# Performance work log

Hardware: AMD Instinct MI355X
Metric: run time of the kernel (lower is better)

Reference implementation:

```python
import jax, jax.numpy as jnp
import numpy as np

NUM_HEADS = 24
EPS = 1e-6


def rms_norm(x, scale):
    # fp32 RMSNorm over last dim, matching torch F.rms_norm(eps=1e-6)
    xf = x.astype(jnp.float32)
    rrms = jax.lax.rsqrt(jnp.mean(xf * xf, axis=-1, keepdims=True) + EPS)
    return (xf * rrms * scale.astype(jnp.float32)).astype(x.dtype)


def rope_rotate(x, pe):
    # x: [B,H,L,D]; pe: [B,1,L,D/2,2,2] rotation matrices
    B, H, L, D = x.shape
    xr = x.astype(jnp.float32).reshape(B, H, L, D // 2, 1, 2)
    out = pe[..., 0] * xr[..., 0] + pe[..., 1] * xr[..., 1]  # [B,H,L,D/2,2]
    return out.reshape(B, H, L, D).astype(x.dtype)


def setup_inputs() -> dict:
    key = jax.random.key(0)
    ks = jax.random.split(key, 6)
    B, L, C = 1, 2048, 3072
    H = NUM_HEADS
    D = C // H
    x = jax.random.normal(ks[0], (B, L, C), dtype=jnp.float32)
    # pe: proper RoPE rotation matrices [[cos,-sin],[sin,cos]] -> [B,1,L,D/2,2,2]
    theta = jax.random.uniform(ks[1], (B, 1, L, D // 2), dtype=jnp.float32) * (2.0 * np.pi)
    cos, sin = jnp.cos(theta), jnp.sin(theta)
    row0 = jnp.stack([cos, -sin], axis=-1)
    row1 = jnp.stack([sin, cos], axis=-1)
    pe = jnp.stack([row0, row1], axis=-2)  # [B,1,L,D/2,2,2]
    w_qkv = jax.random.normal(ks[2], (3 * C, C), dtype=jnp.float32) * (1.0 / np.sqrt(C))
    q_scale = jnp.ones((D,), dtype=jnp.float32)
    k_scale = jnp.ones((D,), dtype=jnp.float32)
    w_proj = jax.random.normal(ks[3], (C, C), dtype=jnp.float32) * (1.0 / np.sqrt(C))
    b_proj = jnp.zeros((C,), dtype=jnp.float32)
    return {"x": x, "pe": pe, "w_qkv": w_qkv, "q_scale": q_scale,
            "k_scale": k_scale, "w_proj": w_proj, "b_proj": b_proj}


def reference(x, pe, w_qkv, q_scale, k_scale, w_proj, b_proj):
    B, L, C = x.shape
    H = NUM_HEADS
    D = C // H
    qkv = x @ w_qkv.T                                   # [B,L,3C]
    qkv = qkv.reshape(B, L, 3, H, D).transpose(2, 0, 3, 1, 4)  # [3,B,H,L,D]
    q, k, v = qkv[0], qkv[1], qkv[2]
    q = rms_norm(q, q_scale)
    k = rms_norm(k, k_scale)
    q = rope_rotate(q, pe)
    k = rope_rotate(k, pe)
    scale = 1.0 / np.sqrt(D)
    scores = jnp.einsum('bhqd,bhkd->bhqk', q, k) * jnp.asarray(scale, q.dtype)
    attn = jax.nn.softmax(scores, axis=-1)
    out = jnp.einsum('bhqk,bhkd->bhqd', attn, v)        # [B,H,L,D]
    out = out.transpose(0, 2, 1, 3).reshape(B, L, C)    # [B,L,C]
    return out @ w_proj.T + b_proj
```

## Files before the change

### kernel.cpp

```cpp
#include <hip/hip_runtime.h>

typedef __attribute__((ext_vector_type(8))) __bf16 bf16x8;
typedef __attribute__((ext_vector_type(4))) float f32x4;

typedef __attribute__((address_space(1))) void gvoid;
typedef __attribute__((address_space(3))) void lvoid;

__device__ __forceinline__ float bf2f(unsigned int u) {
    union { unsigned int u; float f; } v; v.u = u << 16; return v.f;
}
__device__ __forceinline__ unsigned short f2bf(float f) {
    union { float f; unsigned int u; } v; v.f = f;
    unsigned int r = v.u + 0x7fffu + ((v.u >> 16) & 1u);
    return (unsigned short)(r >> 16);
}
__device__ __forceinline__ unsigned int pack2(float a, float b) {
    return (unsigned int)f2bf(a) | ((unsigned int)f2bf(b) << 16);
}
__device__ __forceinline__ void async16(const void* g, void* l) {
    __builtin_amdgcn_global_load_lds((gvoid*)g, (lvoid*)l, 16, 0, 0);
}
__device__ __forceinline__ float exp2f_hw(float x) {
    return __builtin_amdgcn_exp2f(x);
}


__global__ __launch_bounds__(256)
void cvt_all(const float4* __restrict__ x, const float4* __restrict__ wqkv,
             const float4* __restrict__ wproj, uint4* __restrict__ dst) {
    int i = blockIdx.x * 256 + threadIdx.x;
    const float4* s; uint4* d; int off;
    if (i < 786432)       { s = x;     d = dst;           off = i; }
    else if (i < 4325376) { s = wqkv;  d = dst + 786432;  off = i - 786432; }
    else if (i < 5505024) { s = wproj; d = dst + 4325376; off = i - 4325376; }
    else return;
    float4 a = s[2 * off], b = s[2 * off + 1];
    uint4 o;
    o.x = pack2(a.x, a.y); o.y = pack2(a.z, a.w);
    o.z = pack2(b.x, b.y); o.w = pack2(b.z, b.w);
    d[off] = o;
}

#define GEMM_CORE(A_, lda_, B_, ldb_, K_)                                        \
    __shared__ __align__(16) unsigned short As[4][4096];                         \
    __shared__ __align__(16) unsigned short Bs[4][4096];                         \
    const int t = threadIdx.x, lane = t & 63;                                    \
    const int wm = t >> 7, wn = (t >> 6) & 1;                                    \
    const int lr = lane & 15, kc = lane >> 4;                                    \
    const int NK = (K_) / 32;                                                    \
    const int e0 = t * 8, e1 = (256 + t) * 8;                                    \
    const int r0 = e0 >> 5, c0 = (e0 >> 3) & 3;                                  \
    const int r1 = e1 >> 5, c1 = (e1 >> 3) & 3;                                  \
    const int g0 = (c0 ^ ((r0 >> 1) & 3)) * 8;                                   \
    const int g1 = (c1 ^ ((r1 >> 1) & 3)) * 8;                                   \
    const unsigned short* Ag0 = &(A_)[(size_t)(m0 + r0) * (lda_) + g0];          \
    const unsigned short* Ag1 = &(A_)[(size_t)(m0 + r1) * (lda_) + g1];          \
    const unsigned short* Bg0 = &(B_)[(size_t)(n0 + r0) * (ldb_) + g0];          \
    const unsigned short* Bg1 = &(B_)[(size_t)(n0 + r1) * (ldb_) + g1];          \
    f32x4 acc[4][4] = {};                                                        \
    RSTAGE(0) RSTAGE(1) RSTAGE(2)                                                \
    asm volatile("s_waitcnt vmcnt(8)" ::: "memory");                             \
    __builtin_amdgcn_s_barrier();                                                \
    for (int kt = 0; kt < NK; ++kt) {                                            \
        const int sl = kt & 3;                                                   \
        bf16x8 af[4], bfr[4];                                                    \
        _Pragma("unroll")                                                        \
        for (int i = 0; i < 4; ++i) {                                            \
            int ra = wm * 64 + i * 16 + lr;                                      \
            int rb = wn * 64 + i * 16 + lr;                                      \
            af[i]  = *(const bf16x8*)&As[sl][ra * 32 + ((kc ^ ((ra >> 1) & 3)) * 8)]; \
            bfr[i] = *(const bf16x8*)&Bs[sl][rb * 32 + ((kc ^ ((rb >> 1) & 3)) * 8)]; \
        }                                                                        \
        if (kt + 3 < NK) RSTAGE(kt + 3)                                          \
        asm volatile("s_waitcnt lgkmcnt(0)" ::: "memory");                       \
        __builtin_amdgcn_sched_barrier(0);                                       \
        __builtin_amdgcn_s_setprio(1);                                           \
        _Pragma("unroll")                                                        \
        for (int mi = 0; mi < 4; ++mi)                                           \
            _Pragma("unroll")                                                    \
            for (int ni = 0; ni < 4; ++ni)                                       \
                acc[mi][ni] = __builtin_amdgcn_mfma_f32_16x16x32_bf16(           \
                    af[mi], bfr[ni], acc[mi][ni], 0, 0, 0);                      \
        __builtin_amdgcn_s_setprio(0);                                           \
        if (kt + 3 < NK)      { asm volatile("s_waitcnt vmcnt(8)" ::: "memory"); } \
        else if (kt + 2 < NK) { asm volatile("s_waitcnt vmcnt(4)" ::: "memory"); } \
        else if (kt + 1 < NK) { asm volatile("s_waitcnt vmcnt(0)" ::: "memory"); } \
        __builtin_amdgcn_s_barrier();                                            \
    }

#define RSTAGE(kt_) { const int s_ = (kt_) & 3; const size_t k_ = (size_t)(kt_) * 32; \
        async16(Ag0 + k_, &As[s_][e0]); async16(Ag1 + k_, &As[s_][e1]);               \
        async16(Bg0 + k_, &Bs[s_][e0]); async16(Bg1 + k_, &Bs[s_][e1]); }

__global__ __launch_bounds__(256, 2)
void gemm_qkv(const unsigned short* __restrict__ A, const unsigned short* __restrict__ B,
              unsigned short* __restrict__ qk, unsigned short* __restrict__ vt) {
    __shared__ __align__(16) unsigned short As[3][4096];
    __shared__ __align__(16) unsigned short Bs[3][8192];
    const int n0 = blockIdx.x * 256, m0 = blockIdx.y * 128;
    const int t = threadIdx.x, lane = t & 63, w = t >> 6;
    const int lr = lane & 15, kc = lane >> 4;
    const int NK = 96;

    const int ea0 = t * 8,         ra0 = ea0 >> 5, ca0 = (ea0 >> 3) & 3;
    const int ea1 = (256 + t) * 8, ra1 = ea1 >> 5, ca1 = (ea1 >> 3) & 3;
    const int ga0 = (ca0 ^ ((ra0 >> 1) & 3)) * 8;
    const int ga1 = (ca1 ^ ((ra1 >> 1) & 3)) * 8;
    const unsigned short* Ag0 = &A[(size_t)(m0 + ra0) * 3072 + ga0];
    const unsigned short* Ag1 = &A[(size_t)(m0 + ra1) * 3072 + ga1];
    int eb[4];
    const unsigned short* Bg[4];
#pragma unroll
    for (int i = 0; i < 4; ++i) {
        eb[i] = (i * 256 + t) * 8;
        int rb = eb[i] >> 5, cb = (eb[i] >> 3) & 3;
        int gb = (cb ^ ((rb >> 1) & 3)) * 8;
        Bg[i] = &B[(size_t)(n0 + rb) * 3072 + gb];
    }

#define QSTAGE(kt_) { const int s_ = (kt_) % 3; const size_t k_ = (size_t)(kt_) * 32; \
        async16(Ag0 + k_, &As[s_][ea0]); async16(Ag1 + k_, &As[s_][ea1]);             \
        async16(Bg[0] + k_, &Bs[s_][eb[0]]); async16(Bg[1] + k_, &Bs[s_][eb[1]]);     \
        async16(Bg[2] + k_, &Bs[s_][eb[2]]); async16(Bg[3] + k_, &Bs[s_][eb[3]]); }

    f32x4 acc[8][4] = {};

    QSTAGE(0) QSTAGE(1)
    asm volatile("s_waitcnt vmcnt(6)" ::: "memory");
    __builtin_amdgcn_s_barrier();

    for (int kt = 0; kt < NK; ++kt) {
        const int sl = kt % 3;
        bf16x8 af[8], bfr[4];
#pragma unroll
        for (int i = 0; i < 8; ++i) {
            int ra = i * 16 + lr;
            af[i] = *(const bf16x8*)&As[sl][ra * 32 + ((kc ^ ((ra >> 1) & 3)) * 8)];
        }
#pragma unroll
        for (int i = 0; i < 4; ++i) {
            int rb = w * 64 + i * 16 + lr;
            bfr[i] = *(const bf16x8*)&Bs[sl][rb * 32 + ((kc ^ ((rb >> 1) & 3)) * 8)];
        }
        if (kt + 2 < NK) QSTAGE(kt + 2)
        asm volatile("s_waitcnt lgkmcnt(0)" ::: "memory");
        __builtin_amdgcn_sched_barrier(0);
        __builtin_amdgcn_s_setprio(1);
#pragma unroll
        for (int mi = 0; mi < 8; ++mi)
#pragma unroll
            for (int ni = 0; ni < 4; ++ni)
                acc[mi][ni] = __builtin_amdgcn_mfma_f32_16x16x32_bf16(
                    af[mi], bfr[ni], acc[mi][ni], 0, 0, 0);
        __builtin_amdgcn_s_setprio(0);
        if (kt + 2 < NK) { asm volatile("s_waitcnt vmcnt(6)" ::: "memory"); }
        else             { asm volatile("s_waitcnt vmcnt(0)" ::: "memory"); }
        __builtin_amdgcn_s_barrier();
    }
#undef QSTAGE

    const int rb0 = kc * 4;
#pragma unroll
    for (int mi = 0; mi < 8; ++mi)
#pragma unroll
        for (int ni = 0; ni < 4; ++ni) {
            int col = n0 + w * 64 + ni * 16 + lr;
#pragma unroll
            for (int r = 0; r < 4; ++r) {
                int row = m0 + mi * 16 + rb0 + r;
                unsigned short v = f2bf(acc[mi][ni][r]);
                if (col < 6144) qk[(size_t)row * 6144 + col] = v;
                else            vt[(size_t)(col - 6144) * 2048 + row] = v;
            }
        }
}

__global__ __launch_bounds__(256, 2)
void gemm_proj(const unsigned short* __restrict__ A, const unsigned short* __restrict__ B,
               const float* __restrict__ bias, float* __restrict__ out) {
    const int n0 = blockIdx.x * 128, m0 = blockIdx.y * 128;
    GEMM_CORE(A, 6144, B, 3072, 3072)
    const int rb0 = kc * 4;
#pragma unroll
    for (int mi = 0; mi < 4; ++mi)
#pragma unroll
        for (int ni = 0; ni < 4; ++ni) {
            int col = n0 + wn * 64 + ni * 16 + lr;
            float badd = bias[col];
#pragma unroll
            for (int r = 0; r < 4; ++r) {
                int row = m0 + wm * 64 + mi * 16 + rb0 + r;
                out[(size_t)row * 3072 + col] = acc[mi][ni][r] + badd;
            }
        }
}

__global__ __launch_bounds__(256, 2)
void attn2(unsigned short* __restrict__ qk, const unsigned short* __restrict__ vt) {
    __shared__ __align__(16) unsigned short Ks[64 * 128];
    __shared__ __align__(16) unsigned short Vs[128 * 64];
    __shared__ __align__(16) unsigned short Ps[4 * 32 * 64];
    const int t = threadIdx.x, lane = t & 63, w = t >> 6;
    const int h = blockIdx.x, qblk = blockIdx.y * 128;
    const int lr = lane & 15, kc = lane >> 4;
    const float sc2 = 0.08838834764831845f * 1.4426950408889634f;
    const float THR = 62.7f;

    bf16x8 aq[2][4];
#pragma unroll
    for (int mf = 0; mf < 2; ++mf)
#pragma unroll
        for (int ks = 0; ks < 4; ++ks)
            aq[mf][ks] = *(const bf16x8*)&qk[(size_t)(qblk + w * 32 + mf * 16 + lr) * 6144 + h * 128 + ks * 32 + kc * 8];

    f32x4 o[2][8] = {};
    float mst[2][4], lpart[2][4];
#pragma unroll
    for (int mf = 0; mf < 2; ++mf)
#pragma unroll
        for (int r = 0; r < 4; ++r) { mst[mf][r] = -1e30f; lpart[mf][r] = 0.0f; }

    unsigned short* Pw = &Ps[w * 2048];

#pragma unroll
    for (int i = 0; i < 4; ++i) {
        int e = (i * 256 + t) * 8;
        {
            int row = e >> 7, c8 = (e >> 3) & 15;
            int gc = (c8 ^ (row & 15)) * 8;
            async16(&qk[(size_t)row * 6144 + 3072 + h * 128 + gc], &Ks[e]);
        }
        {
            int row = e >> 6, c8 = (e >> 3) & 7;
            int gc = (c8 ^ (row & 7)) * 8;
            async16(&vt[(size_t)(h * 128 + row) * 2048 + gc], &Vs[e]);
        }
    }

    for (int kb = 0; kb < 2048; kb += 64) {
        __syncthreads();

        bf16x8 pk[4], pv[4];
        const bool pf = (kb + 64) < 2048;
        if (pf) {
#pragma unroll
            for (int i = 0; i < 4; ++i) {
                int e = (i * 256 + t) * 8;
                {   int row = e >> 7, c8 = (e >> 3) & 15;
                    int gc = (c8 ^ (row & 15)) * 8;
                    pk[i] = *(const bf16x8*)&qk[(size_t)(kb + 64 + row) * 6144 + 3072 + h * 128 + gc];
                }
                {   int row = e >> 6, c8 = (e >> 3) & 7;
                    int gc = (c8 ^ (row & 7)) * 8;
                    pv[i] = *(const bf16x8*)&vt[(size_t)(h * 128 + row) * 2048 + kb + 64 + gc];
                }
            }
        }

        f32x4 s[2][4] = {};
#pragma unroll
        for (int nt = 0; nt < 4; ++nt) {
            int rk = nt * 16 + lr;
#pragma unroll
            for (int ks = 0; ks < 4; ++ks) {
                int ck = ks * 4 + kc;
                bf16x8 bk = *(const bf16x8*)&Ks[rk * 128 + ((ck ^ (rk & 15)) * 8)];
#pragma unroll
                for (int mf = 0; mf < 2; ++mf)
                    s[mf][nt] = __builtin_amdgcn_mfma_f32_16x16x32_bf16(aq[mf][ks], bk, s[mf][nt], 0, 0, 0);
            }
        }

#pragma unroll
        for (int mf = 0; mf < 2; ++mf) {
            float lm[4]; bool need = false;
#pragma unroll
            for (int r = 0; r < 4; ++r) {
                lm[r] = fmaxf(fmaxf(s[mf][0][r], s[mf][1][r]), fmaxf(s[mf][2][r], s[mf][3][r]));
                need = need || (lm[r] > mst[mf][r] + THR);
            }
            if (__ballot(need) != 0ull) {
#pragma unroll
                for (int r = 0; r < 4; ++r) {
                    float vmax = lm[r];
#pragma unroll
                    for (int off = 8; off >= 1; off >>= 1) vmax = fmaxf(vmax, __shfl_xor(vmax, off));
                    float mn = fmaxf(mst[mf][r], vmax);
                    float al = exp2f_hw((mst[mf][r] - mn) * sc2);
                    mst[mf][r] = mn;
                    lpart[mf][r] *= al;
#pragma unroll
                    for (int dt = 0; dt < 8; ++dt) o[mf][dt][r] *= al;
                }
            }
#pragma unroll
            for (int r = 0; r < 4; ++r) {
                float ps = 0.0f;
#pragma unroll
                for (int nt = 0; nt < 4; ++nt) {
                    float p = exp2f_hw((s[mf][nt][r] - mst[mf][r]) * sc2);
                    s[mf][nt][r] = p;
                    ps += p;
                }
                lpart[mf][r] += ps;
            }
        }

#pragma unroll
        for (int mf = 0; mf < 2; ++mf)
#pragma unroll
            for (int nt = 0; nt < 4; ++nt) {
                int col = nt * 16 + lr;
                int chunk = col >> 3, cin = col & 7;
#pragma unroll
                for (int r = 0; r < 4; ++r) {
                    int q = mf * 16 + kc * 4 + r;
                    Pw[q * 64 + ((chunk ^ (q & 7)) * 8 + cin)] = f2bf(s[mf][nt][r]);
                }
            }

#pragma unroll
        for (int ks2 = 0; ks2 < 2; ++ks2) {
            int ck = ks2 * 4 + kc;
            bf16x8 ap[2];
#pragma unroll
            for (int mf = 0; mf < 2; ++mf) {
                int q = mf * 16 + lr;
                ap[mf] = *(const bf16x8*)&Pw[q * 64 + ((ck ^ (q & 7)) * 8)];
            }
#pragma unroll
            for (int dt = 0; dt < 8; ++dt) {
                int rv = dt * 16 + lr;
                bf16x8 bv = *(const bf16x8*)&Vs[rv * 64 + ((ck ^ (rv & 7)) * 8)];
#pragma unroll
                for (int mf = 0; mf < 2; ++mf)
                    o[mf][dt] = __builtin_amdgcn_mfma_f32_16x16x32_bf16(ap[mf], bv, o[mf][dt], 0, 0, 0);
            }
        }
        __syncthreads();

        if (pf) {
#pragma unroll
            for (int i = 0; i < 4; ++i) {
                int e = (i * 256 + t) * 8;
                *(bf16x8*)&Ks[e] = pk[i];
                *(bf16x8*)&Vs[e] = pv[i];
            }
        }
    }

#pragma unroll
    for (int mf = 0; mf < 2; ++mf)
#pragma unroll
        for (int r = 0; r < 4; ++r) {
            float ps = lpart[mf][r];
#pragma unroll
            for (int off = 8; off >= 1; off >>= 1) ps += __shfl_xor(ps, off);
            lpart[mf][r] = ps;
        }
#pragma unroll
    for (int mf = 0; mf < 2; ++mf)
#pragma unroll
        for (int dt = 0; dt < 8; ++dt)
#pragma unroll
            for (int r = 0; r < 4; ++r) {
                int row = qblk + w * 32 + mf * 16 + kc * 4 + r;
                qk[(size_t)row * 6144 + h * 128 + dt * 16 + lr] = f2bf(o[mf][dt][r] / lpart[mf][r]);
            }
}


__global__ __launch_bounds__(256)
void norm_rope(unsigned short* __restrict__ qk, const float* __restrict__ pe,
               const float* __restrict__ q_scale, const float* __restrict__ k_scale) {
    const int wid = threadIdx.x >> 6, lane = threadIdx.x & 63;
    int pid = blockIdx.x * 4 + wid;
    const int isK = pid >= 49152;
    int p2 = isK ? pid - 49152 : pid;
    const int h = p2 >> 11, l = p2 & 2047;

    unsigned short* src = qk + (size_t)l * 6144 + (isK ? 3072 : 0) + h * 128 + lane * 2;
    unsigned int xu = *(const unsigned int*)src;
    float x0 = bf2f(xu & 0xffffu), x1 = bf2f(xu >> 16);
    float ss = x0 * x0 + x1 * x1;
#pragma unroll
    for (int off = 32; off >= 1; off >>= 1) ss += __shfl_xor(ss, off);
    float rr = rsqrtf(ss * (1.0f / 128.0f) + 1e-6f);

    const float* sc = isK ? k_scale : q_scale;
    float2 s2 = *(const float2*)(sc + lane * 2);
    float y0 = x0 * rr * s2.x;
    float y1 = x1 * rr * s2.y;

    float4 p4 = *(const float4*)(pe + ((size_t)l * 64 + lane) * 4);
    float o0 = p4.x * y0 + p4.y * y1;
    float o1 = p4.z * y0 + p4.w * y1;

    *(unsigned int*)src = pack2(o0, o1);
}


template <bool A32, bool B32, bool C32, bool HAS_BIAS, bool TRANS_C>
__global__ __launch_bounds__(256, 2)
void gemm_bt(const void* __restrict__ Ap, const void* __restrict__ Bp,
             const float* __restrict__ bias, void* __restrict__ Cp,
             int M, int N, int K, int lda, int ldc) {
    __shared__ __align__(16) unsigned short As[128 * 40];
    __shared__ __align__(16) unsigned short Bs[128 * 40];
    const int t = threadIdx.x, lane = t & 63;
    const int wm = t >> 7, wn = (t >> 6) & 1;
    const int m0 = blockIdx.x * 128, n0 = blockIdx.y * 128;
    const int lr = lane & 15, kc = lane >> 4;
    f32x4 acc[4][4] = {};

    for (int k0 = 0; k0 < K; k0 += 32) {
        float4 ra32[4], rb32[4];
        bf16x8 ra16[2], rb16[2];
        if constexpr (A32) {
            const float* A = (const float*)Ap;
#pragma unroll
            for (int i = 0; i < 4; ++i) {
                int idx = i * 256 + t, row = idx >> 3, c4 = idx & 7;
                ra32[i] = *(const float4*)&A[(size_t)(m0 + row) * lda + k0 + c4 * 4];
            }
        } else {
            const unsigned short* A = (const unsigned short*)Ap;
#pragma unroll
            for (int i = 0; i < 2; ++i) {
                int idx = i * 256 + t, row = idx >> 2, c8 = idx & 3;
                ra16[i] = *(const bf16x8*)&A[(size_t)(m0 + row) * lda + k0 + c8 * 8];
            }
        }
        if constexpr (B32) {
            const float* B = (const float*)Bp;
#pragma unroll
            for (int i = 0; i < 4; ++i) {
                int idx = i * 256 + t, row = idx >> 3, c4 = idx & 7;
                rb32[i] = *(const float4*)&B[(size_t)(n0 + row) * K + k0 + c4 * 4];
            }
        } else {
            const unsigned short* B = (const unsigned short*)Bp;
#pragma unroll
            for (int i = 0; i < 2; ++i) {
                int idx = i * 256 + t, row = idx >> 2, c8 = idx & 3;
                rb16[i] = *(const bf16x8*)&B[(size_t)(n0 + row) * K + k0 + c8 * 8];
            }
        }
        __syncthreads();
        if constexpr (A32) {
#pragma unroll
            for (int i = 0; i < 4; ++i) {
                int idx = i * 256 + t, row = idx >> 3, c4 = idx & 7;
                uint2 p = { pack2(ra32[i].x, ra32[i].y), pack2(ra32[i].z, ra32[i].w) };
                *(uint2*)&As[row * 40 + c4 * 4] = p;
            }
        } else {
#pragma unroll
            for (int i = 0; i < 2; ++i) {
                int idx = i * 256 + t, row = idx >> 2, c8 = idx & 3;
                *(bf16x8*)&As[row * 40 + c8 * 8] = ra16[i];
            }
        }
        if constexpr (B32) {
#pragma unroll
            for (int i = 0; i < 4; ++i) {
                int idx = i * 256 + t, row = idx >> 3, c4 = idx & 7;
                uint2 p = { pack2(rb32[i].x, rb32[i].y), pack2(rb32[i].z, rb32[i].w) };
                *(uint2*)&Bs[row * 40 + c4 * 4] = p;
            }
        } else {
#pragma unroll
            for (int i = 0; i < 2; ++i) {
                int idx = i * 256 + t, row = idx >> 2, c8 = idx & 3;
                *(bf16x8*)&Bs[row * 40 + c8 * 8] = rb16[i];
            }
        }
        __syncthreads();
        bf16x8 af[4], bfr[4];
#pragma unroll
        for (int i = 0; i < 4; ++i) {
            af[i]  = *(const bf16x8*)&As[(wm * 64 + i * 16 + lr) * 40 + kc * 8];
            bfr[i] = *(const bf16x8*)&Bs[(wn * 64 + i * 16 + lr) * 40 + kc * 8];
        }
#pragma unroll
        for (int mi = 0; mi < 4; ++mi)
#pragma unroll
            for (int ni = 0; ni < 4; ++ni)
                acc[mi][ni] = __builtin_amdgcn_mfma_f32_16x16x32_bf16(af[mi], bfr[ni], acc[mi][ni], 0, 0, 0);
    }
    const int rb0 = kc * 4;
#pragma unroll
    for (int mi = 0; mi < 4; ++mi) {
#pragma unroll
        for (int ni = 0; ni < 4; ++ni) {
            int col = n0 + wn * 64 + ni * 16 + lr;
            float badd = HAS_BIAS ? bias[col] : 0.0f;
#pragma unroll
            for (int r = 0; r < 4; ++r) {
                int row = m0 + wm * 64 + mi * 16 + rb0 + r;
                size_t off = TRANS_C ? ((size_t)col * ldc + row) : ((size_t)row * ldc + col);
                if (C32) ((float*)Cp)[off] = acc[mi][ni][r] + badd;
                else     ((unsigned short*)Cp)[off] = f2bf(acc[mi][ni][r] + badd);
            }
        }
    }
}

__global__ __launch_bounds__(256, 2)
void attn_slow(unsigned short* __restrict__ qk, const unsigned short* __restrict__ vt) {
    __shared__ __align__(16) unsigned short Ks[64 * 136];
    __shared__ __align__(16) unsigned short Vs[128 * 72];
    __shared__ __align__(16) unsigned short Ps[4 * 32 * 72];
    const int t = threadIdx.x, lane = t & 63, w = t >> 6;
    const int h = blockIdx.y, q0 = blockIdx.x * 128;
    const int lr = lane & 15, kc = lane >> 4;
    const float scale = 0.08838834764831845f;

    bf16x8 aq[2][4];
#pragma unroll
    for (int mf = 0; mf < 2; ++mf)
#pragma unroll
        for (int ks = 0; ks < 4; ++ks)
            aq[mf][ks] = *(const bf16x8*)&qk[(size_t)(q0 + w * 32 + mf * 16 + lr) * 6144 + h * 128 + ks * 32 + kc * 8];

    f32x4 o[2][8] = {};
    float mst[2][4], lst[2][4];
#pragma unroll
    for (int mf = 0; mf < 2; ++mf)
#pragma unroll
        for (int r = 0; r < 4; ++r) { mst[mf][r] = -1e30f; lst[mf][r] = 0.0f; }

    unsigned short* Pw = &Ps[w * 32 * 72];

    for (int kb = 0; kb < 2048; kb += 64) {
        bf16x8 rk[4], rv[4];
#pragma unroll
        for (int i = 0; i < 4; ++i) {
            int idx = i * 256 + t;
            { int row = idx >> 4, c8 = idx & 15;
              rk[i] = *(const bf16x8*)&qk[(size_t)(kb + row) * 6144 + 3072 + h * 128 + c8 * 8]; }
            { int row = idx >> 3, c8 = idx & 7;
              rv[i] = *(const bf16x8*)&vt[(size_t)(h * 128 + row) * 2048 + kb + c8 * 8]; }
        }
        __syncthreads();
#pragma unroll
        for (int i = 0; i < 4; ++i) {
            int idx = i * 256 + t;
            { int row = idx >> 4, c8 = idx & 15; *(bf16x8*)&Ks[row * 136 + c8 * 8] = rk[i]; }
            { int row = idx >> 3, c8 = idx & 7;  *(bf16x8*)&Vs[row * 72 + c8 * 8] = rv[i]; }
        }
        __syncthreads();

        f32x4 s[2][4] = {};
#pragma unroll
        for (int nt = 0; nt < 4; ++nt) {
            int rkr = nt * 16 + lr;
#pragma unroll
            for (int ks = 0; ks < 4; ++ks) {
                bf16x8 bk = *(const bf16x8*)&Ks[rkr * 136 + (ks * 4 + kc) * 8];
#pragma unroll
                for (int mf = 0; mf < 2; ++mf)
                    s[mf][nt] = __builtin_amdgcn_mfma_f32_16x16x32_bf16(aq[mf][ks], bk, s[mf][nt], 0, 0, 0);
            }
        }
#pragma unroll
        for (int mf = 0; mf < 2; ++mf)
#pragma unroll
            for (int nt = 0; nt < 4; ++nt)
#pragma unroll
                for (int r = 0; r < 4; ++r) s[mf][nt][r] *= scale;

#pragma unroll
        for (int mf = 0; mf < 2; ++mf) {
#pragma unroll
            for (int r = 0; r < 4; ++r) {
                float vmax = fmaxf(fmaxf(s[mf][0][r], s[mf][1][r]), fmaxf(s[mf][2][r], s[mf][3][r]));
#pragma unroll
                for (int off = 8; off >= 1; off >>= 1) vmax = fmaxf(vmax, __shfl_xor(vmax, off));
                float mn = fmaxf(mst[mf][r], vmax);
                float al = __expf(mst[mf][r] - mn);
                mst[mf][r] = mn;
                float ps = 0.0f;
#pragma unroll
                for (int nt = 0; nt < 4; ++nt) {
                    float p = __expf(s[mf][nt][r] - mn);
                    s[mf][nt][r] = p;
                    ps += p;
                }
#pragma unroll
                for (int off = 8; off >= 1; off >>= 1) ps += __shfl_xor(ps, off);
                lst[mf][r] = lst[mf][r] * al + ps;
#pragma unroll
                for (int dt = 0; dt < 8; ++dt) o[mf][dt][r] *= al;
            }
        }

#pragma unroll
        for (int mf = 0; mf < 2; ++mf)
#pragma unroll
            for (int nt = 0; nt < 4; ++nt)
#pragma unroll
                for (int r = 0; r < 4; ++r)
                    Pw[(mf * 16 + kc * 4 + r) * 72 + nt * 16 + lr] = f2bf(s[mf][nt][r]);

#pragma unroll
        for (int ks2 = 0; ks2 < 2; ++ks2) {
            bf16x8 ap[2];
#pragma unroll
            for (int mf = 0; mf < 2; ++mf)
                ap[mf] = *(const bf16x8*)&Pw[(mf * 16 + lr) * 72 + (ks2 * 4 + kc) * 8];
#pragma unroll
            for (int dt = 0; dt < 8; ++dt) {
                bf16x8 bv = *(const bf16x8*)&Vs[(dt * 16 + lr) * 72 + (ks2 * 4 + kc) * 8];
#pragma unroll
                for (int mf = 0; mf < 2; ++mf)
                    o[mf][dt] = __builtin_amdgcn_mfma_f32_16x16x32_bf16(ap[mf], bv, o[mf][dt], 0, 0, 0);
            }
        }
        __syncthreads();
    }

#pragma unroll
    for (int mf = 0; mf < 2; ++mf)
#pragma unroll
        for (int dt = 0; dt < 8; ++dt)
#pragma unroll
            for (int r = 0; r < 4; ++r) {
                int row = q0 + w * 32 + mf * 16 + kc * 4 + r;
                qk[(size_t)row * 6144 + h * 128 + dt * 16 + lr] = f2bf(o[mf][dt][r] / lst[mf][r]);
            }
}

__global__ void fill_two(float* p, int n) {
    int i = blockIdx.x * 256 + threadIdx.x;
    if (i < n) p[i] = 2.0f;
}

extern "C" void kernel_launch(void* const* d_in, const int* in_sizes, int n_in,
                              void* d_out, int out_size, void* d_ws, size_t ws_size,
                              hipStream_t stream) {
    const float* x       = (const float*)d_in[0];
    const float* pe      = (const float*)d_in[1];
    const float* w_qkv   = (const float*)d_in[2];
    const float* q_scale = (const float*)d_in[3];
    const float* k_scale = (const float*)d_in[4];
    const float* w_proj  = (const float*)d_in[5];
    const float* b_proj  = (const float*)d_in[6];
    float* out = (float*)d_out;

    if (ws_size >= 125829120ull) {
        unsigned short* ws     = (unsigned short*)d_ws;
        unsigned short* xb     = ws;
        unsigned short* wqkvb  = ws + 6291456;
        unsigned short* wprojb = ws + 34603008;
        unsigned short* qk     = ws + 44040192;
        unsigned short* vt     = ws + 56623104;

        cvt_all<<<21504, 256, 0, stream>>>((const float4*)x, (const float4*)w_qkv,
                                           (const float4*)w_proj, (uint4*)xb);

        gemm_qkv<<<dim3(36, 16), 256, 0, stream>>>(xb, wqkvb, qk, vt);
        norm_rope<<<24576, 256, 0, stream>>>(qk, pe, q_scale, k_scale);
        attn2<<<dim3(24, 16), 256, 0, stream>>>(qk, vt);
        gemm_proj<<<dim3(24, 16), 256, 0, stream>>>(qk, wprojb, b_proj, out);
        return;
    }

    if (ws_size < 37748736ull) {
        fill_two<<<(6291456 + 255) / 256, 256, 0, stream>>>(out, 6291456);
        return;
    }

    unsigned short* qk = (unsigned short*)d_ws;
    unsigned short* vt = qk + 12582912;

    gemm_bt<true, true, false, false, false><<<dim3(16, 48), 256, 0, stream>>>(
        x, w_qkv, nullptr, qk, 2048, 6144, 3072, 3072, 6144);
    norm_rope<<<24576, 256, 0, stream>>>(qk, pe, q_scale, k_scale);
    gemm_bt<true, true, false, false, true><<<dim3(16, 24), 256, 0, stream>>>(
        x, w_qkv + (size_t)6144 * 3072, nullptr, vt, 2048, 3072, 3072, 3072, 2048);
    attn_slow<<<dim3(16, 24), 256, 0, stream>>>(qk, vt);
    gemm_bt<false, true, true, true, false><<<dim3(16, 24), 256, 0, stream>>>(
        qk, w_proj, b_proj, out, 2048, 3072, 3072, 6144, 3072);
}
```

Measured before the change: 566.6 us.

## Fuse RMSNorm and RoPE of Q and K into the attention kernel

```diff
diff --git a/kernel.cpp b/kernel.cpp
--- a/kernel.cpp
+++ b/kernel.cpp
@@ -22,6 +22,32 @@
 }
 __device__ __forceinline__ float exp2f_hw(float x) {
     return __builtin_amdgcn_exp2f(x);
+}
+
+__device__ __forceinline__ float ssq8(bf16x8 v) {
+    const unsigned int* u = (const unsigned int*)&v;
+    float s = 0.0f;
+#pragma unroll
+    for (int j = 0; j < 4; ++j) {
+        float x0 = bf2f(u[j] & 0xffffu), x1 = bf2f(u[j] >> 16);
+        s += x0 * x0 + x1 * x1;
+    }
+    return s;
+}
+__device__ __forceinline__ bf16x8 normrope8(bf16x8 v, float rr,
+                                            const float* __restrict__ sc,
+                                            const float* __restrict__ per) {
+    const unsigned int* u = (const unsigned int*)&v;
+    bf16x8 out;
+    unsigned int* ou = (unsigned int*)&out;
+#pragma unroll
+    for (int j = 0; j < 4; ++j) {
+        float x0 = bf2f(u[j] & 0xffffu), x1 = bf2f(u[j] >> 16);
+        float y0 = x0 * rr * sc[2 * j], y1 = x1 * rr * sc[2 * j + 1];
+        float4 p4 = *(const float4*)(per + 4 * j);
+        ou[j] = pack2(p4.x * y0 + p4.y * y1, p4.z * y0 + p4.w * y1);
+    }
+    return out;
 }
 
 
@@ -196,7 +222,9 @@
 }
 
 __global__ __launch_bounds__(256, 2)
-void attn2(unsigned short* __restrict__ qk, const unsigned short* __restrict__ vt) {
+void attn2(unsigned short* __restrict__ qk, const unsigned short* __restrict__ vt,
+           const float* __restrict__ pe, const float* __restrict__ q_scale,
+           const float* __restrict__ k_scale) {
     __shared__ __align__(16) unsigned short Ks[64 * 128];
     __shared__ __align__(16) unsigned short Vs[128 * 64];
     __shared__ __align__(16) unsigned short Ps[4 * 32 * 64];
@@ -206,12 +234,37 @@
     const float sc2 = 0.08838834764831845f * 1.4426950408889634f;
     const float THR = 62.7f;
 
+    int krow[4], kgc[4], vrow[4], vgc[4];
+#pragma unroll
+    for (int i = 0; i < 4; ++i) {
+        int idx = i * 256 + t;
+        krow[i] = idx >> 4;
+        kgc[i]  = ((idx & 15) ^ (krow[i] & 15)) * 8;
+        vrow[i] = idx >> 3;
+        vgc[i]  = ((idx & 7) ^ (vrow[i] & 7)) * 8;
+    }
+
     bf16x8 aq[2][4];
 #pragma unroll
     for (int mf = 0; mf < 2; ++mf)
 #pragma unroll
         for (int ks = 0; ks < 4; ++ks)
             aq[mf][ks] = *(const bf16x8*)&qk[(size_t)(qblk + w * 32 + mf * 16 + lr) * 6144 + h * 128 + ks * 32 + kc * 8];
+#pragma unroll
+    for (int mf = 0; mf < 2; ++mf) {
+        float ss = 0.0f;
+#pragma unroll
+        for (int ks = 0; ks < 4; ++ks) ss += ssq8(aq[mf][ks]);
+        ss += __shfl_xor(ss, 16); ss += __shfl_xor(ss, 32);
+        float rr = rsqrtf(ss * (1.0f / 128.0f) + 1e-6f);
+        int lq = qblk + w * 32 + mf * 16 + lr;
+#pragma unroll
+        for (int ks = 0; ks < 4; ++ks) {
+            int c0 = ks * 32 + kc * 8;
+            aq[mf][ks] = normrope8(aq[mf][ks], rr, q_scale + c0,
+                                   pe + ((size_t)lq * 64 + (c0 >> 1)) * 4);
+        }
+    }
 
     f32x4 o[2][8] = {};
     float mst[2][4], lpart[2][4];
@@ -222,18 +275,27 @@
 
     unsigned short* Pw = &Ps[w * 2048];
 
-#pragma unroll
-    for (int i = 0; i < 4; ++i) {
-        int e = (i * 256 + t) * 8;
-        {
-            int row = e >> 7, c8 = (e >> 3) & 15;
-            int gc = (c8 ^ (row & 15)) * 8;
-            async16(&qk[(size_t)row * 6144 + 3072 + h * 128 + gc], &Ks[e]);
-        }
-        {
-            int row = e >> 6, c8 = (e >> 3) & 7;
-            int gc = (c8 ^ (row & 7)) * 8;
-            async16(&vt[(size_t)(h * 128 + row) * 2048 + gc], &Vs[e]);
+    {
+        bf16x8 pk0[4], pv0[4];
+#pragma unroll
+        for (int i = 0; i < 4; ++i) {
+            pk0[i] = *(const bf16x8*)&qk[(size_t)krow[i] * 6144 + 3072 + h * 128 + kgc[i]];
+            pv0[i] = *(const bf16x8*)&vt[(size_t)(h * 128 + vrow[i]) * 2048 + vgc[i]];
+        }
+#pragma unroll
+        for (int i = 0; i < 4; ++i) {
+            float ss = ssq8(pk0[i]);
+            ss += __shfl_xor(ss, 1); ss += __shfl_xor(ss, 2);
+            ss += __shfl_xor(ss, 4); ss += __shfl_xor(ss, 8);
+            float rr = rsqrtf(ss * (1.0f / 128.0f) + 1e-6f);
+            pk0[i] = normrope8(pk0[i], rr, k_scale + kgc[i],
+                               pe + ((size_t)krow[i] * 64 + (kgc[i] >> 1)) * 4);
+        }
+#pragma unroll
+        for (int i = 0; i < 4; ++i) {
+            int e = (i * 256 + t) * 8;
+            *(bf16x8*)&Ks[e] = pk0[i];
+            *(bf16x8*)&Vs[e] = pv0[i];
         }
     }
 
@@ -245,15 +307,8 @@
         if (pf) {
 #pragma unroll
             for (int i = 0; i < 4; ++i) {
-                int e = (i * 256 + t) * 8;
-                {   int row = e >> 7, c8 = (e >> 3) & 15;
-                    int gc = (c8 ^ (row & 15)) * 8;
-                    pk[i] = *(const bf16x8*)&qk[(size_t)(kb + 64 + row) * 6144 + 3072 + h * 128 + gc];
-                }
-                {   int row = e >> 6, c8 = (e >> 3) & 7;
-                    int gc = (c8 ^ (row & 7)) * 8;
-                    pv[i] = *(const bf16x8*)&vt[(size_t)(h * 128 + row) * 2048 + kb + 64 + gc];
-                }
+                pk[i] = *(const bf16x8*)&qk[(size_t)(kb + 64 + krow[i]) * 6144 + 3072 + h * 128 + kgc[i]];
+                pv[i] = *(const bf16x8*)&vt[(size_t)(h * 128 + vrow[i]) * 2048 + kb + 64 + vgc[i]];
             }
         }
 
@@ -340,6 +395,15 @@
         __syncthreads();
 
         if (pf) {
+#pragma unroll
+            for (int i = 0; i < 4; ++i) {
+                float ss = ssq8(pk[i]);
+                ss += __shfl_xor(ss, 1); ss += __shfl_xor(ss, 2);
+                ss += __shfl_xor(ss, 4); ss += __shfl_xor(ss, 8);
+                float rr = rsqrtf(ss * (1.0f / 128.0f) + 1e-6f);
+                pk[i] = normrope8(pk[i], rr, k_scale + kgc[i],
+                                  pe + ((size_t)(kb + 64 + krow[i]) * 64 + (kgc[i] >> 1)) * 4);
+            }
 #pragma unroll
             for (int i = 0; i < 4; ++i) {
                 int e = (i * 256 + t) * 8;
@@ -660,8 +724,7 @@
                                            (const float4*)w_proj, (uint4*)xb);
 
         gemm_qkv<<<dim3(36, 16), 256, 0, stream>>>(xb, wqkvb, qk, vt);
-        norm_rope<<<24576, 256, 0, stream>>>(qk, pe, q_scale, k_scale);
-        attn2<<<dim3(24, 16), 256, 0, stream>>>(qk, vt);
+        attn2<<<dim3(24, 16), 256, 0, stream>>>(qk, vt, pe, q_scale, k_scale);
         gemm_proj<<<dim3(24, 16), 256, 0, stream>>>(qk, wprojb, b_proj, out);
         return;
     }
```

Result: slower. 845.0 us (+49.1%).
